# Optimization experiments

Hardware: AMD Instinct MI355X
Metric: run time of the kernel (lower is better)

The kernel has to match this reference:

```python
import jax, jax.numpy as jnp
import numpy as np

N_NODES = 50000
N_EDGES = 625000
D = 128


def setup_inputs() -> dict:
    key = jax.random.key(0)
    kx, ks, kr, kw, kb = jax.random.split(key, 5)
    x = jax.random.normal(kx, (N_NODES, D), dtype=jnp.float32)
    senders = jax.random.randint(ks, (N_EDGES,), 0, N_NODES, dtype=jnp.int64)
    receivers = jax.random.randint(kr, (N_EDGES,), 0, N_NODES, dtype=jnp.int64)
    # nn.Linear(2*D, D): weight [D, 2*D], bias [D]
    lim = 1.0 / np.sqrt(2 * D)
    W = jax.random.uniform(kw, (D, 2 * D), minval=-lim, maxval=lim, dtype=jnp.float32)
    b = jax.random.uniform(kb, (D,), minval=-lim, maxval=lim, dtype=jnp.float32)
    return {"x": x, "senders": senders, "receivers": receivers, "n_nodes": N_NODES, "W": W, "b": b}


def reference(x, senders, receivers, n_nodes, W, b):
    # Add self loops (with_self=True)
    self_idx = jnp.arange(n_nodes, dtype=senders.dtype)
    s = jnp.concatenate([senders, self_idx])   # [E + N]
    r = jnp.concatenate([receivers, self_idx]) # [E + N]

    ones = jnp.ones(r.shape[0], dtype=x.dtype)
    # degree_norm=True branch (note: mirrors the original's naming exactly:
    # 'out_degree' counted over receivers, 'in_degree' over senders)
    out_degree = jax.ops.segment_sum(ones, r, num_segments=n_nodes)  # [N]
    in_degree = jax.ops.segment_sum(ones, s, num_segments=n_nodes)   # [N]
    out_degree_norm = jax.lax.rsqrt(jnp.maximum(out_degree, 1.0))
    in_degree_norm = jax.lax.rsqrt(jnp.maximum(in_degree, 1.0))

    # Gather sender embeddings, scale, scatter-add to receivers
    sender_emb = x[s] * out_degree_norm[s][:, None]  # [E+N, D]
    aggregated = jax.ops.segment_sum(sender_emb, r, num_segments=n_nodes)  # [N, D]

    # edge_count over receivers == out_degree (same scatter), clamped
    edge_count = jnp.maximum(out_degree, 1.0)
    aggregated = aggregated / edge_count[:, None]
    aggregated = aggregated * in_degree_norm[:, None]

    combined = jnp.concatenate([x, aggregated], axis=1)  # [N, 2D]
    return combined @ W.T + b
```

## Files before the change

### kernel.cpp

```cpp
#include <hip/hip_runtime.h>

#define DIM 128
#define BM 128
#define BK 32
#define BINSZ 128
#define EPB 2048

typedef __attribute__((ext_vector_type(8))) short short8;
typedef __attribute__((ext_vector_type(4))) float f32x4;

__device__ __forceinline__ unsigned short f2bf(float f) {
    unsigned int b = __float_as_uint(f);
    return (unsigned short)((b + 0x7fffu + ((b >> 16) & 1u)) >> 16);
}
__device__ __forceinline__ float bf_lo(unsigned int u) { return __uint_as_float(u << 16); }
__device__ __forceinline__ float bf_hi(unsigned int u) { return __uint_as_float(u & 0xffff0000u); }
__device__ __forceinline__ unsigned int pack2(float a, float b) {
    return (unsigned int)f2bf(a) | ((unsigned int)f2bf(b) << 16);
}
__device__ __forceinline__ uint2 pack4(float4 v) {
    uint2 r; r.x = pack2(v.x, v.y); r.y = pack2(v.z, v.w); return r;
}

__global__ void convert_kernel(const float4* __restrict__ x4,
                               const float4* __restrict__ W4,
                               uint2* __restrict__ xb4,
                               uint2* __restrict__ Wb4,
                               int nx4, int nw4) {
    int i = blockIdx.x * blockDim.x + threadIdx.x;
    if (i < nx4) xb4[i] = pack4(x4[i]);
    if (i < nw4) Wb4[i] = pack4(W4[i]);
}

__global__ __launch_bounds__(256) void coarse_hist_kernel(
        const int* __restrict__ senders, const int* __restrict__ receivers,
        int* __restrict__ ccr, int* __restrict__ ccs, int E, int nbin) {
    __shared__ int hr[512], hs[512];
    int t = threadIdx.x;
    for (int b = t; b < nbin; b += 256) { hr[b] = 0; hs[b] = 0; }
    __syncthreads();
    int base = blockIdx.x * EPB;
    for (int k = 0; k < EPB; k += 256) {
        int e = base + k + t;
        if (e < E) {
            atomicAdd(&hr[receivers[e] >> 7], 1);
            atomicAdd(&hs[senders[e] >> 7], 1);
        }
    }
    __syncthreads();
    for (int b = t; b < nbin; b += 256) {
        if (hr[b]) atomicAdd(&ccr[b], hr[b]);
        if (hs[b]) atomicAdd(&ccs[b], hs[b]);
    }
}

__global__ __launch_bounds__(512) void coarse_scan_kernel(
        const int* __restrict__ ccr, const int* __restrict__ ccs,
        int* __restrict__ startR, int* __restrict__ startS,
        int* __restrict__ curR, int* __restrict__ curS,
        int* __restrict__ row_start, int nbin, int N, int E) {
    __shared__ int sh[1024];
    int t = threadIdx.x;
    int vr = (t < nbin) ? ccr[t] : 0;
    int vs = (t < nbin) ? ccs[t] : 0;
    sh[t] = vr; sh[512 + t] = vs;
    __syncthreads();
    for (int off = 1; off < 512; off <<= 1) {
        int ur = (t >= off) ? sh[t - off] : 0;
        int us = (t >= off) ? sh[512 + t - off] : 0;
        __syncthreads();
        sh[t] += ur; sh[512 + t] += us;
        __syncthreads();
    }
    if (t < nbin) {
        int er = sh[t] - vr, es = sh[512 + t] - vs;
        startR[t] = er; curR[t] = er;
        startS[t] = es; curS[t] = es;
    }
    if (t == 0) { startR[nbin] = E; startS[nbin] = E; row_start[N] = E; }
}

__global__ __launch_bounds__(256) void coarse_scatter_kernel(
        const int* __restrict__ senders, const int* __restrict__ receivers,
        int* __restrict__ curR, int* __restrict__ curS,
        unsigned int* __restrict__ bucket_r,
        int* __restrict__ bucket_s,
        int E, int nbin) {
    __shared__ int hr[512], hs[512];
    __shared__ int br_[512], bs_[512];
    int t = threadIdx.x;
    for (int b = t; b < nbin; b += 256) { hr[b] = 0; hs[b] = 0; }
    __syncthreads();
    int base = blockIdx.x * EPB;
    for (int k = 0; k < EPB; k += 256) {
        int e = base + k + t;
        if (e < E) {
            atomicAdd(&hr[receivers[e] >> 7], 1);
            atomicAdd(&hs[senders[e] >> 7], 1);
        }
    }
    __syncthreads();
    for (int b = t; b < nbin; b += 256) {
        br_[b] = hr[b] ? atomicAdd(&curR[b], hr[b]) : 0;
        bs_[b] = hs[b] ? atomicAdd(&curS[b], hs[b]) : 0;
    }
    __syncthreads();
    for (int k = 0; k < EPB; k += 256) {
        int e = base + k + t;
        if (e < E) {
            int s = senders[e], r = receivers[e];
            int pr = atomicAdd(&br_[r >> 7], 1);
            bucket_r[pr] = ((unsigned int)(r & 127) << 16) | (unsigned int)s;
            int ps = atomicAdd(&bs_[s >> 7], 1);
            bucket_s[ps] = s;
        }
    }
}

__global__ __launch_bounds__(256) void fine_r_kernel(
        const unsigned int* __restrict__ bucket_r,
        const int* __restrict__ startR,
        int* __restrict__ edge_src,
        int* __restrict__ row_start, int N) {
    __shared__ int fine[BINSZ];
    __shared__ int fstart[BINSZ];
    int b = blockIdx.x, t = threadIdx.x;
    if (t < BINSZ) fine[t] = 0;
    __syncthreads();
    int lo = startR[b], hi = startR[b + 1];
    for (int i = lo + t; i < hi; i += 256)
        atomicAdd(&fine[bucket_r[i] >> 16], 1);
    __syncthreads();
    if (t < BINSZ) fstart[t] = fine[t];
    __syncthreads();
    for (int off = 1; off < BINSZ; off <<= 1) {
        int u = (t < BINSZ && t >= off) ? fstart[t - off] : 0;
        __syncthreads();
        if (t < BINSZ) fstart[t] += u;
        __syncthreads();
    }
    if (t < BINSZ) {
        int excl = fstart[t] - fine[t];
        int node = b * BINSZ + t;
        if (node < N) row_start[node] = lo + excl;
        fstart[t] = excl;
    }
    __syncthreads();
    for (int i = lo + t; i < hi; i += 256) {
        unsigned int u = bucket_r[i];
        int pos = atomicAdd(&fstart[u >> 16], 1);
        edge_src[lo + pos] = (int)(u & 0xFFFFu);
    }
}

__global__ __launch_bounds__(256) void fine_s_kernel(
        const int* __restrict__ bucket_s,
        const int* __restrict__ startS,
        int* __restrict__ cnt_s, int N) {
    __shared__ int fine[BINSZ];
    int b = blockIdx.x, t = threadIdx.x;
    if (t < BINSZ) fine[t] = 0;
    __syncthreads();
    int lo = startS[b], hi = startS[b + 1];
    for (int i = lo + t; i < hi; i += 256)
        atomicAdd(&fine[bucket_s[i] & 127], 1);
    __syncthreads();
    if (t < BINSZ) {
        int node = b * BINSZ + t;
        if (node < N) cnt_s[node] = fine[t];
    }
}

__global__ __launch_bounds__(256) void prescale_kernel(
        const uint2* __restrict__ xb2,
        const int* __restrict__ row_start,
        const int* __restrict__ cnt_s,
        uint2* __restrict__ xs2,
        float* __restrict__ fs, int N) {
    int i = blockIdx.x * blockDim.x + threadIdx.x;
    int n = i >> 5, c = i & 31;
    if (n >= N) return;
    float od = (float)(row_start[n + 1] - row_start[n] + 1);
    float sc = rsqrtf(od);
    uint2 u = xb2[(size_t)n * 32 + c];
    uint2 o;
    o.x = pack2(bf_lo(u.x) * sc, bf_hi(u.x) * sc);
    o.y = pack2(bf_lo(u.y) * sc, bf_hi(u.y) * sc);
    xs2[(size_t)n * 32 + c] = o;
    if (c == 0) fs[n] = rsqrtf((float)(cnt_s[n] + 1)) / od;
}

__global__ __launch_bounds__(256) void gather_kernel(
        const unsigned int* __restrict__ xs,
        const int* __restrict__ edge_src,
        const int* __restrict__ row_start,
        const float* __restrict__ fs,
        unsigned int* __restrict__ aggb,
        int N) {
    int lane = threadIdx.x & 63;
    int n = (blockIdx.x * blockDim.x + threadIdx.x) >> 6;
    if (n >= N) return;

    int start = row_start[n];
    int deg   = row_start[n + 1] - start;
    float ax = 0.f, ay = 0.f;

    for (int base = 0; base < deg; base += 64) {
        int cnt = deg - base; if (cnt > 64) cnt = 64;
        int src = 0;
        if (lane < cnt) src = edge_src[start + base + lane];
        int j = 0;
        for (; j + 8 <= cnt; j += 8) {
            int ss[8]; unsigned int uu[8];
#pragma unroll
            for (int q = 0; q < 8; q++) ss[q] = __shfl(src, j + q);
#pragma unroll
            for (int q = 0; q < 8; q++) uu[q] = xs[(size_t)ss[q] * 64 + lane];
#pragma unroll
            for (int q = 0; q < 8; q++) { ax += bf_lo(uu[q]); ay += bf_hi(uu[q]); }
        }
        for (; j < cnt; j++) {
            int s = __shfl(src, j);
            unsigned int u = xs[(size_t)s * 64 + lane];
            ax += bf_lo(u); ay += bf_hi(u);
        }
    }

    float f = fs[n];
    unsigned int u = xs[(size_t)n * 64 + lane];
    ax = (ax + bf_lo(u)) * f;
    ay = (ay + bf_hi(u)) * f;
    aggb[(size_t)n * 64 + lane] = pack2(ax, ay);
}

__global__ __launch_bounds__(256) void gemm_kernel(
        const unsigned short* __restrict__ x_bf,
        const unsigned short* __restrict__ agg_bf,
        const unsigned short* __restrict__ W_bf,
        const float* __restrict__ bias,
        float* __restrict__ out, int N) {
    __shared__ unsigned short As[BM * BK];
    __shared__ unsigned short Bs[DIM * BK];

    int t    = threadIdx.x;
    int lane = t & 63;
    int w    = t >> 6;
    int wr   = w >> 1, wc = w & 1;
    int row0 = blockIdx.x * BM;

    f32x4 acc[4][4];
#pragma unroll
    for (int i = 0; i < 4; i++)
#pragma unroll
        for (int j = 0; j < 4; j++) acc[i][j] = (f32x4){0.f, 0.f, 0.f, 0.f};

    for (int kt = 0; kt < 8; kt++) {
        const unsigned short* src = (kt < 4) ? x_bf : agg_bf;
        int k0 = (kt & 3) * BK;
#pragma unroll
        for (int p = 0; p < 2; p++) {
            int idx = p * 256 + t;
            int row = idx >> 2;
            int ch  = idx & 3;
            uint4 v = *(const uint4*)&src[(size_t)(row0 + row) * 128 + k0 + ch * 8];
            *(uint4*)&As[row * BK + ch * 8] = v;
        }
#pragma unroll
        for (int p = 0; p < 2; p++) {
            int idx = p * 256 + t;
            int n   = idx >> 2;
            int ch  = idx & 3;
            uint4 v = *(const uint4*)&W_bf[(size_t)n * 256 + kt * BK + ch * 8];
            *(uint4*)&Bs[n * BK + ch * 8] = v;
        }
        __syncthreads();

        short8 a[4], b[4];
#pragma unroll
        for (int i = 0; i < 4; i++)
            a[i] = *(const short8*)&As[(wr * 64 + i * 16 + (lane & 15)) * BK + (lane >> 4) * 8];
#pragma unroll
        for (int j = 0; j < 4; j++)
            b[j] = *(const short8*)&Bs[(wc * 64 + j * 16 + (lane & 15)) * BK + (lane >> 4) * 8];
#pragma unroll
        for (int i = 0; i < 4; i++)
#pragma unroll
            for (int j = 0; j < 4; j++)
                acc[i][j] = __builtin_amdgcn_mfma_f32_16x16x32_bf16(a[i], b[j], acc[i][j], 0, 0, 0);
        __syncthreads();
    }

    int cq = lane >> 4;
    int cl = lane & 15;
#pragma unroll
    for (int j = 0; j < 4; j++) {
        int col = wc * 64 + j * 16 + cl;
        float bb = bias[col];
#pragma unroll
        for (int i = 0; i < 4; i++) {
            int rbase = row0 + wr * 64 + i * 16 + cq * 4;
#pragma unroll
            for (int r = 0; r < 4; r++) {
                int row = rbase + r;
                if (row < N) out[(size_t)row * DIM + col] = acc[i][j][r] + bb;
            }
        }
    }
}

extern "C" void kernel_launch(void* const* d_in, const int* in_sizes, int n_in,
                              void* d_out, int out_size, void* d_ws, size_t ws_size,
                              hipStream_t stream) {
    const float* x         = (const float*)d_in[0];
    const int*   senders   = (const int*)d_in[1];
    const int*   receivers = (const int*)d_in[2];
    const float* W         = (const float*)d_in[4];
    const float* bias      = (const float*)d_in[5];
    float*       out       = (float*)d_out;

    int N    = in_sizes[0] / DIM;
    int E    = in_sizes[1];
    int nbin = (N + BINSZ - 1) / BINSZ;
    int NAB  = (E + EPB - 1) / EPB;
    int NP   = ((N + BM - 1) / BM) * BM;

    char* ws = (char*)d_ws;
    size_t off = 0;
    #define WS_ALLOC(ptrtype, name, bytes) \
        ptrtype name = (ptrtype)(ws + off); off += (((size_t)(bytes)) + 255) & ~(size_t)255;
    WS_ALLOC(int*,            ccr,       (size_t)nbin * 4)
    WS_ALLOC(int*,            ccs,       (size_t)nbin * 4)
    size_t zero_end = off;
    WS_ALLOC(int*,            startR,    (size_t)(nbin + 1) * 4)
    WS_ALLOC(int*,            startS,    (size_t)(nbin + 1) * 4)
    WS_ALLOC(int*,            curR,      (size_t)nbin * 4)
    WS_ALLOC(int*,            curS,      (size_t)nbin * 4)
    WS_ALLOC(int*,            row_start, (size_t)(N + 1) * 4)
    WS_ALLOC(int*,            cnt_s,     (size_t)N * 4)
    WS_ALLOC(float*,          fs,        (size_t)N * 4)
    WS_ALLOC(int*,            edge_src,  (size_t)E * 4)
    WS_ALLOC(unsigned short*, x_bf,      (size_t)NP * DIM * 2)
    WS_ALLOC(unsigned short*, xs_bf,     (size_t)NP * DIM * 2)
    WS_ALLOC(unsigned short*, agg_bf,    (size_t)NP * DIM * 2)
    WS_ALLOC(unsigned short*, W_bf,      (size_t)DIM * 256 * 2)
    #undef WS_ALLOC

    unsigned int* bucket_r = (unsigned int*)agg_bf;
    int*          bucket_s = (int*)((char*)agg_bf + (((size_t)E * 4 + 255) & ~(size_t)255));

    hipMemsetAsync(ws, 0, zero_end, stream);

    int nx4 = N * 32;
    int nw4 = DIM * 256 / 4;
    convert_kernel<<<(nx4 + 255) / 256, 256, 0, stream>>>(
        (const float4*)x, (const float4*)W, (uint2*)x_bf, (uint2*)W_bf, nx4, nw4);
    coarse_hist_kernel<<<NAB, 256, 0, stream>>>(senders, receivers, ccr, ccs, E, nbin);
    coarse_scan_kernel<<<1, 512, 0, stream>>>(ccr, ccs, startR, startS,
                                              curR, curS, row_start, nbin, N, E);
    coarse_scatter_kernel<<<NAB, 256, 0, stream>>>(senders, receivers, curR, curS,
                                                   bucket_r, bucket_s, E, nbin);
    fine_r_kernel<<<nbin, 256, 0, stream>>>(bucket_r, startR, edge_src, row_start, N);
    fine_s_kernel<<<nbin, 256, 0, stream>>>(bucket_s, startS, cnt_s, N);
    prescale_kernel<<<(N * 32 + 255) / 256, 256, 0, stream>>>(
        (const uint2*)x_bf, row_start, cnt_s, (uint2*)xs_bf, fs, N);
    gather_kernel<<<(N * 64 + 255) / 256, 256, 0, stream>>>(
        (const unsigned int*)xs_bf, edge_src, row_start, fs,
        (unsigned int*)agg_bf, N);
    gemm_kernel<<<(N + BM - 1) / BM, 256, 0, stream>>>(
        x_bf, agg_bf, W_bf, bias, out, N);
}
```

Before: 181.7 us.

## Replace atomic bin counters with per-block histogram scan, fuse fine passes, widen GEMM

The coarse sort now stores each block's histogram and scans it per bin, so the scatter kernel no longer recounts edges or uses global atomics. It also removes the memset. The fine receiver pass, the sender count and the x prescale are merged into one kernel per bin, which drops two launches and the cnt_s buffer. The GEMM moves to 512 threads with 8 waves, each computing a 64x32 tile. This adds a per-bin scan kernel and more histogram memory traffic, and halves MFMA work per wave.

```diff
diff --git a/kernel.cpp b/kernel.cpp
--- a/kernel.cpp
+++ b/kernel.cpp
@@ -32,9 +32,9 @@
     if (i < nw4) Wb4[i] = pack4(W4[i]);
 }
 
-__global__ __launch_bounds__(256) void coarse_hist_kernel(
+__global__ __launch_bounds__(256) void hist_kernel(
         const int* __restrict__ senders, const int* __restrict__ receivers,
-        int* __restrict__ ccr, int* __restrict__ ccs, int E, int nbin) {
+        int* __restrict__ Hr, int* __restrict__ Hs, int E, int nbin) {
     __shared__ int hr[512], hs[512];
     int t = threadIdx.x;
     for (int b = t; b < nbin; b += 256) { hr[b] = 0; hs[b] = 0; }
@@ -48,63 +48,76 @@
         }
     }
     __syncthreads();
+    size_t ho = (size_t)blockIdx.x * nbin;
     for (int b = t; b < nbin; b += 256) {
-        if (hr[b]) atomicAdd(&ccr[b], hr[b]);
-        if (hs[b]) atomicAdd(&ccs[b], hs[b]);
-    }
-}
-
-__global__ __launch_bounds__(512) void coarse_scan_kernel(
-        const int* __restrict__ ccr, const int* __restrict__ ccs,
-        int* __restrict__ startR, int* __restrict__ startS,
-        int* __restrict__ curR, int* __restrict__ curS,
+        Hr[ho + b] = hr[b];
+        Hs[ho + b] = hs[b];
+    }
+}
+
+__global__ __launch_bounds__(512) void scan_bins_kernel(
+        int* __restrict__ Hr, int* __restrict__ Hs,
+        int* __restrict__ tot_r, int* __restrict__ tot_s,
+        int NAB, int nbin) {
+    __shared__ int sr[512], ss[512];
+    int b = blockIdx.x, t = threadIdx.x;
+    int vr = (t < NAB) ? Hr[(size_t)t * nbin + b] : 0;
+    int vs = (t < NAB) ? Hs[(size_t)t * nbin + b] : 0;
+    sr[t] = vr; ss[t] = vs;
+    __syncthreads();
+    for (int off = 1; off < 512; off <<= 1) {
+        int ur = (t >= off) ? sr[t - off] : 0;
+        int us = (t >= off) ? ss[t - off] : 0;
+        __syncthreads();
+        sr[t] += ur; ss[t] += us;
+        __syncthreads();
+    }
+    if (t < NAB) {
+        Hr[(size_t)t * nbin + b] = sr[t] - vr;
+        Hs[(size_t)t * nbin + b] = ss[t] - vs;
+    }
+    if (t == 511) { tot_r[b] = sr[511]; tot_s[b] = ss[511]; }
+}
+
+__global__ __launch_bounds__(512) void scan_base_kernel(
+        const int* __restrict__ tot_r, const int* __restrict__ tot_s,
+        int* __restrict__ base_r, int* __restrict__ base_s,
         int* __restrict__ row_start, int nbin, int N, int E) {
-    __shared__ int sh[1024];
+    __shared__ int sr[512], ss[512];
     int t = threadIdx.x;
-    int vr = (t < nbin) ? ccr[t] : 0;
-    int vs = (t < nbin) ? ccs[t] : 0;
-    sh[t] = vr; sh[512 + t] = vs;
+    int vr = (t < nbin) ? tot_r[t] : 0;
+    int vs = (t < nbin) ? tot_s[t] : 0;
+    sr[t] = vr; ss[t] = vs;
     __syncthreads();
     for (int off = 1; off < 512; off <<= 1) {
-        int ur = (t >= off) ? sh[t - off] : 0;
-        int us = (t >= off) ? sh[512 + t - off] : 0;
-        __syncthreads();
-        sh[t] += ur; sh[512 + t] += us;
+        int ur = (t >= off) ? sr[t - off] : 0;
+        int us = (t >= off) ? ss[t - off] : 0;
+        __syncthreads();
+        sr[t] += ur; ss[t] += us;
         __syncthreads();
     }
     if (t < nbin) {
-        int er = sh[t] - vr, es = sh[512 + t] - vs;
-        startR[t] = er; curR[t] = er;
-        startS[t] = es; curS[t] = es;
-    }
-    if (t == 0) { startR[nbin] = E; startS[nbin] = E; row_start[N] = E; }
-}
-
-__global__ __launch_bounds__(256) void coarse_scatter_kernel(
+        base_r[t] = sr[t] - vr;
+        base_s[t] = ss[t] - vs;
+    }
+    if (t == 0) { base_r[nbin] = E; base_s[nbin] = E; row_start[N] = E; }
+}
+
+__global__ __launch_bounds__(256) void scatter_kernel(
         const int* __restrict__ senders, const int* __restrict__ receivers,
-        int* __restrict__ curR, int* __restrict__ curS,
-        unsigned int* __restrict__ bucket_r,
-        int* __restrict__ bucket_s,
+        const int* __restrict__ Hr, const int* __restrict__ Hs,
+        const int* __restrict__ base_r, const int* __restrict__ base_s,
+        unsigned int* __restrict__ bucket_r, int* __restrict__ bucket_s,
         int E, int nbin) {
-    __shared__ int hr[512], hs[512];
     __shared__ int br_[512], bs_[512];
     int t = threadIdx.x;
-    for (int b = t; b < nbin; b += 256) { hr[b] = 0; hs[b] = 0; }
+    size_t ho = (size_t)blockIdx.x * nbin;
+    for (int b = t; b < nbin; b += 256) {
+        br_[b] = base_r[b] + Hr[ho + b];
+        bs_[b] = base_s[b] + Hs[ho + b];
+    }
     __syncthreads();
     int base = blockIdx.x * EPB;
-    for (int k = 0; k < EPB; k += 256) {
-        int e = base + k + t;
-        if (e < E) {
-            atomicAdd(&hr[receivers[e] >> 7], 1);
-            atomicAdd(&hs[senders[e] >> 7], 1);
-        }
-    }
-    __syncthreads();
-    for (int b = t; b < nbin; b += 256) {
-        br_[b] = hr[b] ? atomicAdd(&curR[b], hr[b]) : 0;
-        bs_[b] = hs[b] ? atomicAdd(&curS[b], hs[b]) : 0;
-    }
-    __syncthreads();
     for (int k = 0; k < EPB; k += 256) {
         int e = base + k + t;
         if (e < E) {
@@ -117,20 +130,31 @@
     }
 }
 
-__global__ __launch_bounds__(256) void fine_r_kernel(
+__global__ __launch_bounds__(256) void fine_kernel(
         const unsigned int* __restrict__ bucket_r,
-        const int* __restrict__ startR,
+        const int* __restrict__ bucket_s,
+        const int* __restrict__ base_r,
+        const int* __restrict__ base_s,
+        const uint2* __restrict__ xb2,
         int* __restrict__ edge_src,
-        int* __restrict__ row_start, int N) {
-    __shared__ int fine[BINSZ];
-    __shared__ int fstart[BINSZ];
+        int* __restrict__ row_start,
+        float* __restrict__ fs,
+        uint2* __restrict__ xs2,
+        int N) {
+    __shared__ int fine[BINSZ], fstart[BINSZ], cs[BINSZ];
+    __shared__ float scs[BINSZ];
     int b = blockIdx.x, t = threadIdx.x;
-    if (t < BINSZ) fine[t] = 0;
-    __syncthreads();
-    int lo = startR[b], hi = startR[b + 1];
-    for (int i = lo + t; i < hi; i += 256)
+    if (t < BINSZ) { fine[t] = 0; cs[t] = 0; }
+    __syncthreads();
+
+    int loR = base_r[b], hiR = base_r[b + 1];
+    int loS = base_s[b], hiS = base_s[b + 1];
+    for (int i = loR + t; i < hiR; i += 256)
         atomicAdd(&fine[bucket_r[i] >> 16], 1);
-    __syncthreads();
+    for (int i = loS + t; i < hiS; i += 256)
+        atomicAdd(&cs[bucket_s[i] & 127], 1);
+    __syncthreads();
+
     if (t < BINSZ) fstart[t] = fine[t];
     __syncthreads();
     for (int off = 1; off < BINSZ; off <<= 1) {
@@ -142,52 +166,36 @@
     if (t < BINSZ) {
         int excl = fstart[t] - fine[t];
         int node = b * BINSZ + t;
-        if (node < N) row_start[node] = lo + excl;
+        float od = (float)(fine[t] + 1);
+        float sc = rsqrtf(od);
+        scs[t] = sc;
+        if (node < N) {
+            row_start[node] = loR + excl;
+            fs[node] = rsqrtf((float)(cs[t] + 1)) / od;
+        }
         fstart[t] = excl;
     }
     __syncthreads();
-    for (int i = lo + t; i < hi; i += 256) {
+
+    for (int i = loR + t; i < hiR; i += 256) {
         unsigned int u = bucket_r[i];
         int pos = atomicAdd(&fstart[u >> 16], 1);
-        edge_src[lo + pos] = (int)(u & 0xFFFFu);
-    }
-}
-
-__global__ __launch_bounds__(256) void fine_s_kernel(
-        const int* __restrict__ bucket_s,
-        const int* __restrict__ startS,
-        int* __restrict__ cnt_s, int N) {
-    __shared__ int fine[BINSZ];
-    int b = blockIdx.x, t = threadIdx.x;
-    if (t < BINSZ) fine[t] = 0;
-    __syncthreads();
-    int lo = startS[b], hi = startS[b + 1];
-    for (int i = lo + t; i < hi; i += 256)
-        atomicAdd(&fine[bucket_s[i] & 127], 1);
-    __syncthreads();
-    if (t < BINSZ) {
-        int node = b * BINSZ + t;
-        if (node < N) cnt_s[node] = fine[t];
-    }
-}
-
-__global__ __launch_bounds__(256) void prescale_kernel(
-        const uint2* __restrict__ xb2,
-        const int* __restrict__ row_start,
-        const int* __restrict__ cnt_s,
-        uint2* __restrict__ xs2,
-        float* __restrict__ fs, int N) {
-    int i = blockIdx.x * blockDim.x + threadIdx.x;
-    int n = i >> 5, c = i & 31;
-    if (n >= N) return;
-    float od = (float)(row_start[n + 1] - row_start[n] + 1);
-    float sc = rsqrtf(od);
-    uint2 u = xb2[(size_t)n * 32 + c];
-    uint2 o;
-    o.x = pack2(bf_lo(u.x) * sc, bf_hi(u.x) * sc);
-    o.y = pack2(bf_lo(u.y) * sc, bf_hi(u.y) * sc);
-    xs2[(size_t)n * 32 + c] = o;
-    if (c == 0) fs[n] = rsqrtf((float)(cnt_s[n] + 1)) / od;
+        edge_src[loR + pos] = (int)(u & 0xFFFFu);
+    }
+
+    int nrow0 = b * BINSZ;
+    for (int idx = t; idx < BINSZ * 32; idx += 256) {
+        int row = idx >> 5, c = idx & 31;
+        int node = nrow0 + row;
+        if (node < N) {
+            float sc = scs[row];
+            uint2 u = xb2[(size_t)node * 32 + c];
+            uint2 o;
+            o.x = pack2(bf_lo(u.x) * sc, bf_hi(u.x) * sc);
+            o.y = pack2(bf_lo(u.y) * sc, bf_hi(u.y) * sc);
+            xs2[(size_t)node * 32 + c] = o;
+        }
+    }
 }
 
 __global__ __launch_bounds__(256) void gather_kernel(
@@ -233,7 +241,7 @@
     aggb[(size_t)n * 64 + lane] = pack2(ax, ay);
 }
 
-__global__ __launch_bounds__(256) void gemm_kernel(
+__global__ __launch_bounds__(512) void gemm_kernel(
         const unsigned short* __restrict__ x_bf,
         const unsigned short* __restrict__ agg_bf,
         const unsigned short* __restrict__ W_bf,
@@ -245,47 +253,41 @@
     int t    = threadIdx.x;
     int lane = t & 63;
     int w    = t >> 6;
-    int wr   = w >> 1, wc = w & 1;
+    int wr   = w >> 2, wc = w & 3;
     int row0 = blockIdx.x * BM;
 
-    f32x4 acc[4][4];
+    f32x4 acc[4][2];
 #pragma unroll
     for (int i = 0; i < 4; i++)
 #pragma unroll
-        for (int j = 0; j < 4; j++) acc[i][j] = (f32x4){0.f, 0.f, 0.f, 0.f};
+        for (int j = 0; j < 2; j++) acc[i][j] = (f32x4){0.f, 0.f, 0.f, 0.f};
 
     for (int kt = 0; kt < 8; kt++) {
         const unsigned short* src = (kt < 4) ? x_bf : agg_bf;
         int k0 = (kt & 3) * BK;
-#pragma unroll
-        for (int p = 0; p < 2; p++) {
-            int idx = p * 256 + t;
-            int row = idx >> 2;
-            int ch  = idx & 3;
+        {
+            int row = t >> 2, ch = t & 3;
             uint4 v = *(const uint4*)&src[(size_t)(row0 + row) * 128 + k0 + ch * 8];
             *(uint4*)&As[row * BK + ch * 8] = v;
         }
-#pragma unroll
-        for (int p = 0; p < 2; p++) {
-            int idx = p * 256 + t;
-            int n   = idx >> 2;
-            int ch  = idx & 3;
+        {
+            int n = t >> 2, ch = t & 3;
             uint4 v = *(const uint4*)&W_bf[(size_t)n * 256 + kt * BK + ch * 8];
             *(uint4*)&Bs[n * BK + ch * 8] = v;
         }
         __syncthreads();
 
-        short8 a[4], b[4];
+        short8 a[4], b[2];
 #pragma unroll
         for (int i = 0; i < 4; i++)
             a[i] = *(const short8*)&As[(wr * 64 + i * 16 + (lane & 15)) * BK + (lane >> 4) * 8];
 #pragma unroll
-        for (int j = 0; j < 4; j++)
-            b[j] = *(const short8*)&Bs[(wc * 64 + j * 16 + (lane & 15)) * BK + (lane >> 4) * 8];
+        for (int j = 0; j < 2; j++)
+            b[j] = *(const short8*)&Bs[(wc * 32 + j * 16 + (lane & 15)) * BK + (lane >> 4) * 8];
 #pragma unroll
         for (int i = 0; i < 4; i++)
 #pragma unroll
-            for (int j = 0; j < 4; j++)
+            for (int j = 0; j < 2; j++)
                 acc[i][j] = __builtin_amdgcn_mfma_f32_16x16x32_bf16(a[i], b[j], acc[i][j], 0, 0, 0);
         __syncthreads();
     }
@@ -293,8 +295,8 @@
     int cq = lane >> 4;
     int cl = lane & 15;
 #pragma unroll
-    for (int j = 0; j < 4; j++) {
-        int col = wc * 64 + j * 16 + cl;
+    for (int j = 0; j < 2; j++) {
+        int col = wc * 32 + j * 16 + cl;
         float bb = bias[col];
 #pragma unroll
         for (int i = 0; i < 4; i++) {
@@ -328,15 +330,11 @@
     size_t off = 0;
     #define WS_ALLOC(ptrtype, name, bytes) \
         ptrtype name = (ptrtype)(ws + off); off += (((size_t)(bytes)) + 255) & ~(size_t)255;
-    WS_ALLOC(int*,            ccr,       (size_t)nbin * 4)
-    WS_ALLOC(int*,            ccs,       (size_t)nbin * 4)
-    size_t zero_end = off;
-    WS_ALLOC(int*,            startR,    (size_t)(nbin + 1) * 4)
-    WS_ALLOC(int*,            startS,    (size_t)(nbin + 1) * 4)
-    WS_ALLOC(int*,            curR,      (size_t)nbin * 4)
-    WS_ALLOC(int*,            curS,      (size_t)nbin * 4)
+    WS_ALLOC(int*,            tot_r,     (size_t)nbin * 4)
+    WS_ALLOC(int*,            tot_s,     (size_t)nbin * 4)
+    WS_ALLOC(int*,            base_r,    (size_t)(nbin + 1) * 4)
+    WS_ALLOC(int*,            base_s,    (size_t)(nbin + 1) * 4)
     WS_ALLOC(int*,            row_start, (size_t)(N + 1) * 4)
-    WS_ALLOC(int*,            cnt_s,     (size_t)N * 4)
     WS_ALLOC(float*,          fs,        (size_t)N * 4)
     WS_ALLOC(int*,            edge_src,  (size_t)E * 4)
     WS_ALLOC(unsigned short*, x_bf,      (size_t)NP * DIM * 2)
@@ -345,27 +343,29 @@
     WS_ALLOC(unsigned short*, W_bf,      (size_t)DIM * 256 * 2)
     #undef WS_ALLOC
 
+    size_t eb = ((size_t)E * 4 + 255) & ~(size_t)255;
+    size_t hb = ((size_t)NAB * nbin * 4 + 255) & ~(size_t)255;
     unsigned int* bucket_r = (unsigned int*)agg_bf;
-    int*          bucket_s = (int*)((char*)agg_bf + (((size_t)E * 4 + 255) & ~(size_t)255));
-
-    hipMemsetAsync(ws, 0, zero_end, stream);
+    int*          bucket_s = (int*)((char*)agg_bf + eb);
+    int*          Hr       = (int*)((char*)agg_bf + 2 * eb);
+    int*          Hs       = (int*)((char*)agg_bf + 2 * eb + hb);
 
     int nx4 = N * 32;
     int nw4 = DIM * 256 / 4;
     convert_kernel<<<(nx4 + 255) / 256, 256, 0, stream>>>(
         (const float4*)x, (const float4*)W, (uint2*)x_bf, (uint2*)W_bf, nx4, nw4);
-    coarse_hist_kernel<<<NAB, 256, 0, stream>>>(senders, receivers, ccr, ccs, E, nbin);
-    coarse_scan_kernel<<<1, 512, 0, stream>>>(ccr, ccs, startR, startS,
-                                              curR, curS, row_start, nbin, N, E);
-    coarse_scatter_kernel<<<NAB, 256, 0, stream>>>(senders, receivers, curR, curS,
-                                                   bucket_r, bucket_s, E, nbin);
-    fine_r_kernel<<<nbin, 256, 0, stream>>>(bucket_r, startR, edge_src, row_start, N);
-    fine_s_kernel<<<nbin, 256, 0, stream>>>(bucket_s, startS, cnt_s, N);
-    prescale_kernel<<<(N * 32 + 255) / 256, 256, 0, stream>>>(
-        (const uint2*)x_bf, row_start, cnt_s, (uint2*)xs_bf, fs, N);
+    hist_kernel<<<NAB, 256, 0, stream>>>(senders, receivers, Hr, Hs, E, nbin);
+    scan_bins_kernel<<<nbin, 512, 0, stream>>>(Hr, Hs, tot_r, tot_s, NAB, nbin);
+    scan_base_kernel<<<1, 512, 0, stream>>>(tot_r, tot_s, base_r, base_s,
+                                            row_start, nbin, N, E);
+    scatter_kernel<<<NAB, 256, 0, stream>>>(senders, receivers, Hr, Hs,
+                                            base_r, base_s, bucket_r, bucket_s, E, nbin);
+    fine_kernel<<<nbin, 256, 0, stream>>>(bucket_r, bucket_s, base_r, base_s,
+                                          (const uint2*)x_bf, edge_src, row_start,
+                                          fs, (uint2*)xs_bf, N);
     gather_kernel<<<(N * 64 + 255) / 256, 256, 0, stream>>>(
         (const unsigned int*)xs_bf, edge_src, row_start, fs,
         (unsigned int*)agg_bf, N);
-    gemm_kernel<<<(N + BM - 1) / BM, 256, 0, stream>>>(
+    gemm_kernel<<<(N + BM - 1) / BM, 512, 0, stream>>>(
         x_bf, agg_bf, W_bf, bias, out, N);
 }
```

Result: faster. 177.7 us (-2.2%).
